# Kernel optimization log

Measured on AMD Instinct MI355X. Metric: run time of the kernel, lower is better.

Reference implementation:

```python
import jax, jax.numpy as jnp
import numpy as np

N = 50000   # input points
E = 800000  # edges
M = 25000   # sampled points (ratio 0.5)
K = 15      # num_neighbors
H = 128     # hidden_dim
BN_EPS = 1e-5


def setup_inputs() -> dict:
    key = jax.random.key(0)
    ks = jax.random.split(key, 16)
    w = lambda k, s: jax.random.normal(k, s, dtype=jnp.float32) * 0.02
    z = lambda s: jnp.zeros(s, jnp.float32)
    o = lambda s: jnp.ones(s, jnp.float32)
    return {
        'points': jax.random.normal(ks[0], (N, 3), jnp.float32),
        'edge_index': jax.random.randint(ks[1], (2, E), 0, N),
        'sampled_idx': jnp.sort(jax.random.randint(ks[2], (M,), 0, N)),
        'neighbors': jax.random.randint(ks[3], (M, K), 0, M),
        'W1': w(ks[4], (3, H)), 'b1': z(H), 'g1': o(H), 'beta1': z(H),
        'W2': w(ks[5], (H, H)), 'b2': z(H), 'g2': o(H), 'beta2': z(H),
        'Wc': w(ks[6], (H, H)), 'bc': z(H),
        'Wn': w(ks[7], (H, H)), 'bn_b': z(H),
        'Wq': w(ks[8], (H, H // 2)), 'bq': z(H // 2),
        'Wk': w(ks[9], (H, H // 2)), 'bk': z(H // 2),
        'Wcat': w(ks[10], (H + 3, H + 3)), 'bcat': z(H + 3),
        'Wout': w(ks[11], (H + 3, 3)), 'bout': z(3),
    }


def _bn(x, g, b):
    # BatchNorm1d in training mode: batch mean, biased batch var
    m = x.mean(axis=0)
    v = x.var(axis=0)
    return g * (x - m) * jax.lax.rsqrt(v + BN_EPS) + b


def reference(points, edge_index, sampled_idx, neighbors,
              W1, b1, g1, beta1, W2, b2, g2, beta2,
              Wc, bc, Wn, bn_b, Wq, bq, Wk, bk, Wcat, bcat, Wout, bout):
    n = points.shape[0]
    # PointMLP x2: Linear -> BN -> ReLU
    x = jax.nn.relu(_bn(points @ W1 + b1, g1, beta1))
    x = jax.nn.relu(_bn(x @ W2 + b2, g2, beta2))
    # CustomGNN: relu(W_c x + mean_{j in N(i)} W_n x_j)
    src, dst = edge_index[0], edge_index[1]
    msg = (x @ Wn + bn_b)[src]                                   # [E, H]
    agg = jax.ops.segment_sum(msg, dst, num_segments=n)          # [N, H]
    cnt = jax.ops.segment_sum(jnp.ones(src.shape, jnp.float32), dst, num_segments=n)
    agg = agg / jnp.maximum(cnt, 1.0)[:, None]
    x = jax.nn.relu(x @ Wc + bc + agg)
    # sampling (indices precomputed, like fps output)
    sp = points[sampled_idx]                                     # [M, 3]
    sx = x[sampled_idx]                                          # [M, H]
    # AttentionLayer, fully vectorized over sampled points
    q = sx @ Wq + bq                                             # [M, H/2]
    nb_x = sx[neighbors]                                         # [M, K, H]
    k = nb_x @ Wk + bk                                           # [M, K, H/2]
    scale = jnp.sqrt(jnp.float32(q.shape[-1])) + 1e-6
    scores = jnp.einsum('md,mkd->mk', q, k) / scale              # [M, K]
    mask = (neighbors != 0).astype(jnp.float32)                  # quirk preserved
    attn = jax.nn.softmax(scores * mask, axis=1)                 # [M, K]
    rel = sp[neighbors] - sp[:, None, :]                         # [M, K, 3]
    cat = jnp.concatenate([nb_x, rel], axis=-1)                  # [M, K, H+3]
    proc = cat @ Wcat + bcat                                     # [M, K, H+3]
    aggf = jnp.einsum('mk,mkd->md', attn, proc)                  # [M, H+3]
    disp = aggf @ Wout + bout                                    # [M, 3]
    refined = sp + disp
    return refined, sx
```

## Files before the change

### kernel.cpp

```cpp
#include <hip/hip_runtime.h>
#include <climits>

#define NPTS 50000
#define NE   800000
#define MS   25000
#define KN   15
#define HD   128

__device__ __forceinline__ float wave_sum(float v) {
#pragma unroll
    for (int o = 32; o > 0; o >>= 1) v += __shfl_xor(v, o, 64);
    return v;
}

__launch_bounds__(256)
__global__ void prep_kernel(const float* __restrict__ Wq, const float* __restrict__ bq,
                            const float* __restrict__ Wk, const float* __restrict__ bk,
                            const float* __restrict__ Wcat, const float* __restrict__ bcat,
                            const float* __restrict__ Wout, const float* __restrict__ bout,
                            const float* __restrict__ Wc, const float* __restrict__ Wn,
                            float* __restrict__ Wqk, float* __restrict__ biasQK,
                            float* __restrict__ WcWn,
                            float* __restrict__ Wco128, float* __restrict__ w3, float* __restrict__ bco) {
    int b = blockIdx.x, tid = threadIdx.x;
    if (b < 64) {
        int i = b * 256 + tid;
        int k = i >> 7, c = i & 127;
        Wqk[i] = (c < 64) ? Wq[k * 64 + c] : Wk[k * 64 + (c - 64)];
    } else if (b < 192) {
        int i = (b - 64) * 256 + tid;
        int k = i >> 7, c = i & 127;
        WcWn[i] = (k < 128) ? Wc[k * 128 + c] : Wn[(k - 128) * 128 + c];
    } else if (b == 192) {
        if (tid < 128) biasQK[tid] = (tid < 64) ? bq[tid] : bk[tid - 64];
    } else {
        int wid = tid >> 6, lane = tid & 63;
        int out = (b - 193) * 4 + wid;
        if (out < 396) {
            int r = out / 3, j = out - r * 3;
            const float* src = (r < 131) ? &Wcat[r * 131] : bcat;
            float s = 0.f;
            s = fmaf(src[lane], Wout[lane * 3 + j], s);
            s = fmaf(src[lane + 64], Wout[(lane + 64) * 3 + j], s);
            if (lane < 3) s = fmaf(src[lane + 128], Wout[(lane + 128) * 3 + j], s);
            s = wave_sum(s);
            if (lane == 0) {
                if (r < 128) Wco128[r * 3 + j] = s;
                else if (r < 131) w3[(r - 128) * 3 + j] = s;
                else bco[j] = s + bout[j];
            }
        }
    }
}

__launch_bounds__(256)
__global__ void lin1_kernel(const float* __restrict__ pts, const float* __restrict__ W1,
                            const float* __restrict__ b1, float* __restrict__ y1,
                            float* __restrict__ psum, float* __restrict__ psq) {
    int c = threadIdx.x & 127;
    int half = threadIdx.x >> 7;
    int part = blockIdx.x * 2 + half;
    float w0 = W1[c], w1 = W1[128 + c], w2 = W1[256 + c], bb = b1[c];
    float s = 0.f, s2 = 0.f;
    int r0 = part * 25, r1 = r0 + 25; if (r1 > NPTS) r1 = NPTS;
    for (int r = r0; r < r1; ++r) {
        float p0 = pts[r * 3], p1 = pts[r * 3 + 1], p2 = pts[r * 3 + 2];
        float y = fmaf(p0, w0, fmaf(p1, w1, fmaf(p2, w2, bb)));
        y1[r * HD + c] = y;
        s += y; s2 = fmaf(y, y, s2);
    }
    psum[part * 128 + c] = s;
    psq[part * 128 + c] = s2;
}

__launch_bounds__(256)
__global__ void bn_fin_par(const float* __restrict__ psum, const float* __restrict__ psq, int nb,
                           const float* __restrict__ g, const float* __restrict__ beta,
                           float* __restrict__ tp) {
    int c = blockIdx.x;
    int t = threadIdx.x;
    float S = 0.f, S2 = 0.f;
    for (int b = t; b < nb; b += 256) {
        S += psum[b * 128 + c];
        S2 += psq[b * 128 + c];
    }
    S = wave_sum(S); S2 = wave_sum(S2);
    __shared__ float sA[4], sB[4];
    int wid = t >> 6, lane = t & 63;
    if (lane == 0) { sA[wid] = S; sB[wid] = S2; }
    __syncthreads();
    if (t == 0) {
        float Sa = sA[0] + sA[1] + sA[2] + sA[3];
        float Sb = sB[0] + sB[1] + sB[2] + sB[3];
        const float invN = 1.f / (float)NPTS;
        float mean = Sa * invN;
        float var = Sb * invN - mean * mean;
        float a = g[c] * rsqrtf(var + 1e-5f);
        tp[c] = a;
        tp[128 + c] = beta[c] - mean * a;
    }
}

#define FMA_BLOCK \
        { float av = a0.x; FMA4(0, w0) } { float av = a0.y; FMA4(0, w1) } \
        { float av = a0.z; FMA4(0, w2) } { float av = a0.w; FMA4(0, w3v) } \
        { float av = a1.x; FMA4(1, w0) } { float av = a1.y; FMA4(1, w1) } \
        { float av = a1.z; FMA4(1, w2) } { float av = a1.w; FMA4(1, w3v) } \
        { float av = a2.x; FMA4(2, w0) } { float av = a2.y; FMA4(2, w1) } \
        { float av = a2.z; FMA4(2, w2) } { float av = a2.w; FMA4(2, w3v) }
#define FMA4(ai, wv) \
        acc[ai][0] = fmaf(av, wv.x, acc[ai][0]); acc[ai][1] = fmaf(av, wv.y, acc[ai][1]); \
        acc[ai][2] = fmaf(av, wv.z, acc[ai][2]); acc[ai][3] = fmaf(av, wv.w, acc[ai][3]);

template <bool TRANS, bool STATS>
__launch_bounds__(256)
__global__ void gemm_bn(const float* __restrict__ A, int nrows,
                        const float* __restrict__ W, const float* __restrict__ bias,
                        const float* __restrict__ tp,
                        float* __restrict__ Out,
                        float* __restrict__ psum, float* __restrict__ psq) {
    __shared__ float As[48][68];
    __shared__ float Ws[64][64];
    int tid = threadIdx.x;
    int cb = blockIdx.x & 1, rb = blockIdx.x >> 1;
    int r0 = rb * 48;
    int tc = tid & 15, tr = tid >> 4;
    int tr3 = tr * 3;
    float acc[3][4] = {};

    for (int k0 = 0; k0 < 128; k0 += 64) {
        if (k0) __syncthreads();
        for (int i = tid; i < 48 * 16; i += 256) {
            int r = i >> 4, c4 = (i & 15) << 2;
            int gr = r0 + r;
            float4 v = make_float4(0.f, 0.f, 0.f, 0.f);
            if (gr < nrows) {
                v = *reinterpret_cast<const float4*>(&A[gr * HD + k0 + c4]);
                if (TRANS) {
                    int gc = k0 + c4;
                    v.x = fmaxf(fmaf(tp[gc],     v.x, tp[128 + gc]),     0.f);
                    v.y = fmaxf(fmaf(tp[gc + 1], v.y, tp[128 + gc + 1]), 0.f);
                    v.z = fmaxf(fmaf(tp[gc + 2], v.z, tp[128 + gc + 2]), 0.f);
                    v.w = fmaxf(fmaf(tp[gc + 3], v.w, tp[128 + gc + 3]), 0.f);
                }
            }
            *reinterpret_cast<float4*>(&As[r][c4]) = v;
        }
        for (int i = tid; i < 64 * 16; i += 256) {
            int k = i >> 4, c4 = (i & 15) << 2;
            *reinterpret_cast<float4*>(&Ws[k][c4]) =
                *reinterpret_cast<const float4*>(&W[(k0 + k) * 128 + (cb << 6) + c4]);
        }
        __syncthreads();
#pragma unroll 2
        for (int k = 0; k < 64; k += 4) {
            const float4 a0 = *reinterpret_cast<const float4*>(&As[tr3][k]);
            const float4 a1 = *reinterpret_cast<const float4*>(&As[tr3 + 1][k]);
            const float4 a2 = *reinterpret_cast<const float4*>(&As[tr3 + 2][k]);
            const float4 w0 = *reinterpret_cast<const float4*>(&Ws[k][tc << 2]);
            const float4 w1 = *reinterpret_cast<const float4*>(&Ws[k + 1][tc << 2]);
            const float4 w2 = *reinterpret_cast<const float4*>(&Ws[k + 2][tc << 2]);
            const float4 w3v = *reinterpret_cast<const float4*>(&Ws[k + 3][tc << 2]);
            FMA_BLOCK
        }
    }

    int c0 = (cb << 6) + (tc << 2);
    float b0 = bias[c0], b1v = bias[c0 + 1], b2v = bias[c0 + 2], b3v = bias[c0 + 3];
    float cs[4] = {}, cq[4] = {};
#pragma unroll
    for (int i = 0; i < 3; ++i) {
        int gr = r0 + tr3 + i;
        float v0 = acc[i][0] + b0, v1 = acc[i][1] + b1v, v2 = acc[i][2] + b2v, v3 = acc[i][3] + b3v;
        if (gr < nrows) {
            *reinterpret_cast<float4*>(&Out[gr * HD + c0]) = make_float4(v0, v1, v2, v3);
            if (STATS) {
                cs[0] += v0; cs[1] += v1; cs[2] += v2; cs[3] += v3;
                cq[0] = fmaf(v0, v0, cq[0]); cq[1] = fmaf(v1, v1, cq[1]);
                cq[2] = fmaf(v2, v2, cq[2]); cq[3] = fmaf(v3, v3, cq[3]);
            }
        }
    }
    if (STATS) {
        float* red = &As[0][0];
        __syncthreads();
        *reinterpret_cast<float4*>(&red[tr * 64 + (tc << 2)]) = make_float4(cs[0], cs[1], cs[2], cs[3]);
        __syncthreads();
        if (tid < 64) {
            float s = 0.f;
            for (int t = 0; t < 16; ++t) s += red[t * 64 + tid];
            psum[rb * 128 + (cb << 6) + tid] = s;
        }
        __syncthreads();
        *reinterpret_cast<float4*>(&red[tr * 64 + (tc << 2)]) = make_float4(cq[0], cq[1], cq[2], cq[3]);
        __syncthreads();
        if (tid < 64) {
            float s = 0.f;
            for (int t = 0; t < 16; ++t) s += red[t * 64 + tid];
            psq[rb * 128 + (cb << 6) + tid] = s;
        }
    }
}

__launch_bounds__(256)
__global__ void init_kernel(int* __restrict__ inv, int* __restrict__ cnt, int* __restrict__ cursor) {
    int i = blockIdx.x * 256 + threadIdx.x;
    if (i < NPTS) inv[i] = INT_MAX;
    if (i < MS) { cnt[i] = 0; cursor[i] = 0; }
}

__launch_bounds__(256)
__global__ void invset_kernel(const int* __restrict__ smp, int* __restrict__ inv) {
    int m = blockIdx.x * 256 + threadIdx.x;
    if (m < MS) atomicMin(&inv[smp[m]], m);
}

__launch_bounds__(256)
__global__ void count_kernel(const int* __restrict__ ei, const int* __restrict__ inv,
                             int* __restrict__ cnt) {
    int e = blockIdx.x * 256 + threadIdx.x;
    if (e < NE) {
        int mr = inv[ei[NE + e]];
        if (mr < MS) atomicAdd(&cnt[mr], 1);
    }
}

__launch_bounds__(1024)
__global__ void scan_kernel(const int* __restrict__ cnt, int* __restrict__ offs) {
    const int C = 25;
    __shared__ int buf[1024];
    int tid = threadIdx.x;
    int loc[C];
    int run = 0;
    int base = tid * C;
#pragma unroll
    for (int i = 0; i < C; ++i) {
        int idx = base + i;
        int v = (idx < MS) ? cnt[idx] : 0;
        loc[i] = run; run += v;
    }
    buf[tid] = run;
    __syncthreads();
    for (int off = 1; off < 1024; off <<= 1) {
        int t = (tid >= off) ? buf[tid - off] : 0;
        __syncthreads();
        buf[tid] += t;
        __syncthreads();
    }
    int excl = buf[tid] - run;
#pragma unroll
    for (int i = 0; i < C; ++i) {
        int idx = base + i;
        if (idx < MS) offs[idx] = excl + loc[i];
    }
    if (tid == 1023) offs[MS] = buf[tid];
}

__launch_bounds__(256)
__global__ void scatter_kernel(const int* __restrict__ ei, const int* __restrict__ inv,
                               const int* __restrict__ offs, int* __restrict__ cursor,
                               int* __restrict__ elist) {
    int e = blockIdx.x * 256 + threadIdx.x;
    if (e < NE) {
        int mr = inv[ei[NE + e]];
        if (mr < MS) {
            int pos = atomicAdd(&cursor[mr], 1);
            elist[offs[mr] + pos] = ei[e];
        }
    }
}

__launch_bounds__(256)
__global__ void agg_kernel(const int* __restrict__ smp, const int* __restrict__ inv,
                           const int* __restrict__ offs, const int* __restrict__ elist,
                           const float* __restrict__ y2, const float* __restrict__ tp2,
                           float* __restrict__ aggX, float* __restrict__ hasE) {
    int tid = threadIdx.x, wid = tid >> 6, lane = tid & 63;
    int m = blockIdx.x * 4 + wid;
    if (m >= MS) return;
    int d = smp[m];
    if (inv[d] != m) return;
    int c0 = lane << 1;
    float ta0 = tp2[c0], ta1 = tp2[c0 + 1];
    float tb0 = tp2[128 + c0], tb1 = tp2[128 + c0 + 1];
    int e0 = offs[m], e1 = offs[m + 1];
    float sx0[8] = {}, sx1[8] = {};
    int e = e0;
    for (; e + 7 < e1; e += 8) {
        float2 v[8];
#pragma unroll
        for (int j = 0; j < 8; ++j)
            v[j] = *reinterpret_cast<const float2*>(&y2[elist[e + j] * HD + c0]);
#pragma unroll
        for (int j = 0; j < 8; ++j) {
            sx0[j] += fmaxf(fmaf(ta0, v[j].x, tb0), 0.f);
            sx1[j] += fmaxf(fmaf(ta1, v[j].y, tb1), 0.f);
        }
    }
    for (; e < e1; ++e) {
        const float2 v = *reinterpret_cast<const float2*>(&y2[elist[e] * HD + c0]);
        sx0[0] += fmaxf(fmaf(ta0, v.x, tb0), 0.f);
        sx1[0] += fmaxf(fmaf(ta1, v.y, tb1), 0.f);
    }
    float s0 = ((sx0[0] + sx0[1]) + (sx0[2] + sx0[3])) + ((sx0[4] + sx0[5]) + (sx0[6] + sx0[7]));
    float s1 = ((sx1[0] + sx1[1]) + (sx1[2] + sx1[3])) + ((sx1[4] + sx1[5]) + (sx1[6] + sx1[7]));
    float rs = 1.f / fmaxf((float)(e1 - e0), 1.f);
    *reinterpret_cast<float2*>(&aggX[m * HD + c0]) = make_float2(s0 * rs, s1 * rs);
    if (lane == 0) hasE[m] = (e1 > e0) ? 1.f : 0.f;
}

__launch_bounds__(256)
__global__ void gemm_sx(const float* __restrict__ y2, const float* __restrict__ aggX,
                        const float* __restrict__ hasE,
                        const int* __restrict__ smp, const int* __restrict__ inv,
                        const float* __restrict__ WcWn,
                        const float* __restrict__ bc, const float* __restrict__ bn_b,
                        const float* __restrict__ tp2,
                        float* __restrict__ sx) {
    __shared__ float As[48][68];
    __shared__ float Ws[64][64];
    int tid = threadIdx.x;
    int cb = blockIdx.x & 1, rb = blockIdx.x >> 1;
    int r0 = rb * 48;
    int tc = tid & 15, tr = tid >> 4;
    int tr3 = tr * 3;
    float acc[3][4] = {};

    for (int kk = 0; kk < 4; ++kk) {
        if (kk) __syncthreads();
        for (int i = tid; i < 48 * 16; i += 256) {
            int r = i >> 4, c4 = (i & 15) << 2;
            int gr = r0 + r;
            float4 v = make_float4(0.f, 0.f, 0.f, 0.f);
            if (gr < MS) {
                int d = smp[gr];
                if (kk < 2) {
                    int gc = (kk << 6) + c4;
                    v = *reinterpret_cast<const float4*>(&y2[d * HD + gc]);
                    v.x = fmaxf(fmaf(tp2[gc],     v.x, tp2[128 + gc]),     0.f);
                    v.y = fmaxf(fmaf(tp2[gc + 1], v.y, tp2[128 + gc + 1]), 0.f);
                    v.z = fmaxf(fmaf(tp2[gc + 2], v.z, tp2[128 + gc + 2]), 0.f);
                    v.w = fmaxf(fmaf(tp2[gc + 3], v.w, tp2[128 + gc + 3]), 0.f);
                } else {
                    v = *reinterpret_cast<const float4*>(&aggX[inv[d] * HD + ((kk - 2) << 6) + c4]);
                }
            }
            *reinterpret_cast<float4*>(&As[r][c4]) = v;
        }
        for (int i = tid; i < 64 * 16; i += 256) {
            int k = i >> 4, c4 = (i & 15) << 2;
            *reinterpret_cast<float4*>(&Ws[k][c4]) =
                *reinterpret_cast<const float4*>(&WcWn[((kk << 6) + k) * 128 + (cb << 6) + c4]);
        }
        __syncthreads();
#pragma unroll 2
        for (int k = 0; k < 64; k += 4) {
            const float4 a0 = *reinterpret_cast<const float4*>(&As[tr3][k]);
            const float4 a1 = *reinterpret_cast<const float4*>(&As[tr3 + 1][k]);
            const float4 a2 = *reinterpret_cast<const float4*>(&As[tr3 + 2][k]);
            const float4 w0 = *reinterpret_cast<const float4*>(&Ws[k][tc << 2]);
            const float4 w1 = *reinterpret_cast<const float4*>(&Ws[k + 1][tc << 2]);
            const float4 w2 = *reinterpret_cast<const float4*>(&Ws[k + 2][tc << 2]);
            const float4 w3v = *reinterpret_cast<const float4*>(&Ws[k + 3][tc << 2]);
            FMA_BLOCK
        }
    }

    int c0 = (cb << 6) + (tc << 2);
    float4 bcv = *reinterpret_cast<const float4*>(&bc[c0]);
    float4 bnv = *reinterpret_cast<const float4*>(&bn_b[c0]);
#pragma unroll
    for (int i = 0; i < 3; ++i) {
        int gr = r0 + tr3 + i;
        if (gr < MS) {
            float f = hasE[inv[smp[gr]]];
            float v0 = fmaxf(acc[i][0] + bcv.x + f * bnv.x, 0.f);
            float v1 = fmaxf(acc[i][1] + bcv.y + f * bnv.y, 0.f);
            float v2 = fmaxf(acc[i][2] + bcv.z + f * bnv.z, 0.f);
            float v3 = fmaxf(acc[i][3] + bcv.w + f * bnv.w, 0.f);
            *reinterpret_cast<float4*>(&sx[gr * HD + c0]) = make_float4(v0, v1, v2, v3);
        }
    }
}

__launch_bounds__(256)
__global__ void p3_kernel(const float* __restrict__ sx, const float* __restrict__ Wco128,
                          const int* __restrict__ smp, const float* __restrict__ pts,
                          float* __restrict__ p3, float* __restrict__ sp) {
    int wid = threadIdx.x >> 6, lane = threadIdx.x & 63;
    int m = blockIdx.x * 4 + wid;
    if (m >= MS) return;
    int c0 = lane << 1;
    const float2 v = *reinterpret_cast<const float2*>(&sx[m * HD + c0]);
    float q0 = v.x * Wco128[c0 * 3]     + v.y * Wco128[(c0 + 1) * 3];
    float q1 = v.x * Wco128[c0 * 3 + 1] + v.y * Wco128[(c0 + 1) * 3 + 1];
    float q2 = v.x * Wco128[c0 * 3 + 2] + v.y * Wco128[(c0 + 1) * 3 + 2];
    q0 = wave_sum(q0); q1 = wave_sum(q1); q2 = wave_sum(q2);
    int d = smp[m];
    if (lane == 0) { p3[m * 3] = q0; p3[m * 3 + 1] = q1; p3[m * 3 + 2] = q2; }
    if (lane < 3) sp[m * 3 + lane] = pts[d * 3 + lane];
}

__launch_bounds__(256)
__global__ void attn_kernel(const float* __restrict__ qk, const int* __restrict__ nbr,
                            const float* __restrict__ p3, const float* __restrict__ sp,
                            const float* __restrict__ w3, const float* __restrict__ bco,
                            float* __restrict__ refined) {
    int wid = threadIdx.x >> 6, lane = threadIdx.x & 63;
    int m = blockIdx.x * 4 + wid;
    if (m >= MS) return;
    float ql = qk[m * HD + lane];
    int nbv[KN];
    float s[KN];
#pragma unroll
    for (int j = 0; j < KN; ++j) nbv[j] = nbr[m * KN + j];
#pragma unroll
    for (int j = 0; j < KN; ++j) {
        float t = ql * qk[nbv[j] * HD + 64 + lane];
        t = wave_sum(t);
        s[j] = (nbv[j] != 0) ? t * (1.f / 8.000001f) : 0.f;
    }
    float mx = s[0];
#pragma unroll
    for (int j = 1; j < KN; ++j) mx = fmaxf(mx, s[j]);
    float den = 0.f;
#pragma unroll
    for (int j = 0; j < KN; ++j) { s[j] = __expf(s[j] - mx); den += s[j]; }
    float invd = 1.f / den;
    float sp0 = sp[m * 3], sp1 = sp[m * 3 + 1], sp2 = sp[m * 3 + 2];
    float a0 = 0.f, a1 = 0.f, a2 = 0.f;
#pragma unroll
    for (int j = 0; j < KN; ++j) {
        int nb = nbv[j];
        float wgt = s[j] * invd;
        float r0 = sp[nb * 3] - sp0, r1 = sp[nb * 3 + 1] - sp1, r2 = sp[nb * 3 + 2] - sp2;
        float g0 = p3[nb * 3]     + r0 * w3[0] + r1 * w3[3] + r2 * w3[6];
        float g1 = p3[nb * 3 + 1] + r0 * w3[1] + r1 * w3[4] + r2 * w3[7];
        float g2 = p3[nb * 3 + 2] + r0 * w3[2] + r1 * w3[5] + r2 * w3[8];
        a0 = fmaf(wgt, g0, a0); a1 = fmaf(wgt, g1, a1); a2 = fmaf(wgt, g2, a2);
    }
    if (lane == 0) {
        refined[m * 3]     = sp0 + a0 + bco[0];
        refined[m * 3 + 1] = sp1 + a1 + bco[1];
        refined[m * 3 + 2] = sp2 + a2 + bco[2];
    }
}

extern "C" void kernel_launch(void* const* d_in, const int* in_sizes, int n_in,
                              void* d_out, int out_size, void* d_ws, size_t ws_size,
                              hipStream_t stream) {
    const float* pts   = (const float*)d_in[0];
    const int*   ei    = (const int*)d_in[1];
    const int*   smp   = (const int*)d_in[2];
    const int*   nbr   = (const int*)d_in[3];
    const float* W1    = (const float*)d_in[4];
    const float* b1    = (const float*)d_in[5];
    const float* g1    = (const float*)d_in[6];
    const float* beta1 = (const float*)d_in[7];
    const float* W2    = (const float*)d_in[8];
    const float* b2    = (const float*)d_in[9];
    const float* g2    = (const float*)d_in[10];
    const float* beta2 = (const float*)d_in[11];
    const float* Wc    = (const float*)d_in[12];
    const float* bc    = (const float*)d_in[13];
    const float* Wn    = (const float*)d_in[14];
    const float* bn_b  = (const float*)d_in[15];
    const float* Wq    = (const float*)d_in[16];
    const float* bq    = (const float*)d_in[17];
    const float* Wk    = (const float*)d_in[18];
    const float* bk    = (const float*)d_in[19];
    const float* Wcat  = (const float*)d_in[20];
    const float* bcat  = (const float*)d_in[21];
    const float* Wout  = (const float*)d_in[22];
    const float* bout  = (const float*)d_in[23];
    (void)in_sizes; (void)n_in; (void)out_size; (void)ws_size;

    float* w = (float*)d_ws;
    size_t o = 0;
    float* y1     = w + o; o += 6400000;
    float* y2     = w + o; o += 6400000;
    float* aggX   = w + o; o += 3200000;
    float* qkb    = w + o; o += 3200000;
    float* psum   = w + o; o += 262144;
    float* psq    = w + o; o += 262144;
    float* tp1    = w + o; o += 256;
    float* tp2    = w + o; o += 256;
    float* Wqk    = w + o; o += 16384;
    float* biasQK = w + o; o += 128;
    float* WcWn   = w + o; o += 32768;
    float* Wco128 = w + o; o += 384;
    float* w3     = w + o; o += 16;
    float* bco    = w + o; o += 16;
    float* p3     = w + o; o += 75008;
    float* sp     = w + o; o += 75008;
    float* hasE   = w + o; o += 25008;
    int* ip    = (int*)(w + o);
    int* inv   = ip;            ip += NPTS;
    int* cnt   = ip;            ip += MS;
    int* cursor= ip;            ip += MS;
    int* offs  = ip;            ip += MS + 4;
    int* elist = ip;

    float* refined = (float*)d_out;
    float* sx      = (float*)d_out + 75000;

    prep_kernel<<<292, 256, 0, stream>>>(Wq, bq, Wk, bk, Wcat, bcat, Wout, bout, Wc, Wn,
                                         Wqk, biasQK, WcWn, Wco128, w3, bco);
    lin1_kernel<<<1000, 256, 0, stream>>>(pts, W1, b1, y1, psum, psq);
    bn_fin_par<<<128, 256, 0, stream>>>(psum, psq, 2000, g1, beta1, tp1);
    gemm_bn<true, true><<<2084, 256, 0, stream>>>(y1, NPTS, W2, b2, tp1, y2, psum, psq);
    bn_fin_par<<<128, 256, 0, stream>>>(psum, psq, 1042, g2, beta2, tp2);
    init_kernel<<<196, 256, 0, stream>>>(inv, cnt, cursor);
    invset_kernel<<<98, 256, 0, stream>>>(smp, inv);
    count_kernel<<<3125, 256, 0, stream>>>(ei, inv, cnt);
    scan_kernel<<<1, 1024, 0, stream>>>(cnt, offs);
    scatter_kernel<<<3125, 256, 0, stream>>>(ei, inv, offs, cursor, elist);
    agg_kernel<<<6250, 256, 0, stream>>>(smp, inv, offs, elist, y2, tp2, aggX, hasE);
    gemm_sx<<<1042, 256, 0, stream>>>(y2, aggX, hasE, smp, inv, WcWn, bc, bn_b, tp2, sx);
    p3_kernel<<<6250, 256, 0, stream>>>(sx, Wco128, smp, pts, p3, sp);
    gemm_bn<false, false><<<1042, 256, 0, stream>>>(sx, MS, Wqk, biasQK, nullptr, qkb,
                                                    nullptr, nullptr);
    attn_kernel<<<6250, 256, 0, stream>>>(qkb, nbr, p3, sp, w3, bco, refined);
}
```

Before: 337.6 us.

## Fuse index-setup kernels into compute launches, widen GEMM tiles, vectorize aggregation

Three small setup kernels are removed by folding their work into extra blocks of existing launches. Buffer init moves into prep_kernel, inverse-map atomicMin into lin1_kernel, and edge counting into the first BN GEMM. The GEMM kernels now compute all 128 output columns per block instead of splitting columns across two blocks, which halves grid size and reuses A tiles at the cost of more registers and LDS. The aggregation kernel splits each wave into two half-waves that each load float4 rows for alternating edges and combine them with a shuffle, improving memory access width.

```diff
diff --git a/kernel.cpp b/kernel.cpp
--- a/kernel.cpp
+++ b/kernel.cpp
@@ -21,7 +21,8 @@
                             const float* __restrict__ Wc, const float* __restrict__ Wn,
                             float* __restrict__ Wqk, float* __restrict__ biasQK,
                             float* __restrict__ WcWn,
-                            float* __restrict__ Wco128, float* __restrict__ w3, float* __restrict__ bco) {
+                            float* __restrict__ Wco128, float* __restrict__ w3, float* __restrict__ bco,
+                            int* __restrict__ inv, int* __restrict__ cnt, int* __restrict__ cursor) {
     int b = blockIdx.x, tid = threadIdx.x;
     if (b < 64) {
         int i = b * 256 + tid;
@@ -33,7 +34,7 @@
         WcWn[i] = (k < 128) ? Wc[k * 128 + c] : Wn[(k - 128) * 128 + c];
     } else if (b == 192) {
         if (tid < 128) biasQK[tid] = (tid < 64) ? bq[tid] : bk[tid - 64];
-    } else {
+    } else if (b < 293) {
         int wid = tid >> 6, lane = tid & 63;
         int out = (b - 193) * 4 + wid;
         if (out < 396) {
@@ -50,13 +51,23 @@
                 else bco[j] = s + bout[j];
             }
         }
+    } else {
+        int i = (b - 293) * 256 + tid;
+        if (i < NPTS) inv[i] = INT_MAX;
+        if (i < MS) { cnt[i] = 0; cursor[i] = 0; }
     }
 }
 
 __launch_bounds__(256)
 __global__ void lin1_kernel(const float* __restrict__ pts, const float* __restrict__ W1,
                             const float* __restrict__ b1, float* __restrict__ y1,
-                            float* __restrict__ psum, float* __restrict__ psq) {
+                            float* __restrict__ psum, float* __restrict__ psq,
+                            const int* __restrict__ smp, int* __restrict__ inv) {
+    if (blockIdx.x >= 1000) {
+        int m = (blockIdx.x - 1000) * 256 + threadIdx.x;
+        if (m < MS) atomicMin(&inv[smp[m]], m);
+        return;
+    }
     int c = threadIdx.x & 127;
     int half = threadIdx.x >> 7;
     int part = blockIdx.x * 2 + half;
@@ -101,32 +112,30 @@
     }
 }
 
-#define FMA_BLOCK \
-        { float av = a0.x; FMA4(0, w0) } { float av = a0.y; FMA4(0, w1) } \
-        { float av = a0.z; FMA4(0, w2) } { float av = a0.w; FMA4(0, w3v) } \
-        { float av = a1.x; FMA4(1, w0) } { float av = a1.y; FMA4(1, w1) } \
-        { float av = a1.z; FMA4(1, w2) } { float av = a1.w; FMA4(1, w3v) } \
-        { float av = a2.x; FMA4(2, w0) } { float av = a2.y; FMA4(2, w1) } \
-        { float av = a2.z; FMA4(2, w2) } { float av = a2.w; FMA4(2, w3v) }
-#define FMA4(ai, wv) \
-        acc[ai][0] = fmaf(av, wv.x, acc[ai][0]); acc[ai][1] = fmaf(av, wv.y, acc[ai][1]); \
-        acc[ai][2] = fmaf(av, wv.z, acc[ai][2]); acc[ai][3] = fmaf(av, wv.w, acc[ai][3]);
-
-template <bool TRANS, bool STATS>
-__launch_bounds__(256)
-__global__ void gemm_bn(const float* __restrict__ A, int nrows,
+template <bool TRANS, bool STATS, bool COUNT>
+__launch_bounds__(256)
+__global__ void gemm_bn(const float* __restrict__ A, int nrows, int gemmBlocks,
                         const float* __restrict__ W, const float* __restrict__ bias,
                         const float* __restrict__ tp,
                         float* __restrict__ Out,
-                        float* __restrict__ psum, float* __restrict__ psq) {
+                        float* __restrict__ psum, float* __restrict__ psq,
+                        const int* __restrict__ ei, const int* __restrict__ inv,
+                        int* __restrict__ cnt) {
+    if (COUNT && (int)blockIdx.x >= gemmBlocks) {
+        int e = ((int)blockIdx.x - gemmBlocks) * 256 + threadIdx.x;
+        if (e < NE) {
+            int mr = inv[ei[NE + e]];
+            if (mr < MS) atomicAdd(&cnt[mr], 1);
+        }
+        return;
+    }
     __shared__ float As[48][68];
-    __shared__ float Ws[64][64];
+    __shared__ float Ws[64][128];
     int tid = threadIdx.x;
-    int cb = blockIdx.x & 1, rb = blockIdx.x >> 1;
-    int r0 = rb * 48;
+    int r0 = blockIdx.x * 48;
     int tc = tid & 15, tr = tid >> 4;
-    int tr3 = tr * 3;
-    float acc[3][4] = {};
+    int tr3 = tr * 3, tc8 = tc << 3;
+    float accA[3][4] = {}, accB[3][4] = {};
 
     for (int k0 = 0; k0 < 128; k0 += 64) {
         if (k0) __syncthreads();
@@ -146,10 +155,10 @@
             }
             *reinterpret_cast<float4*>(&As[r][c4]) = v;
         }
-        for (int i = tid; i < 64 * 16; i += 256) {
-            int k = i >> 4, c4 = (i & 15) << 2;
+        for (int i = tid; i < 64 * 32; i += 256) {
+            int k = i >> 5, c4 = (i & 31) << 2;
             *reinterpret_cast<float4*>(&Ws[k][c4]) =
-                *reinterpret_cast<const float4*>(&W[(k0 + k) * 128 + (cb << 6) + c4]);
+                *reinterpret_cast<const float4*>(&W[(k0 + k) * 128 + c4]);
         }
         __syncthreads();
 #pragma unroll 2
@@ -157,71 +166,73 @@
             const float4 a0 = *reinterpret_cast<const float4*>(&As[tr3][k]);
             const float4 a1 = *reinterpret_cast<const float4*>(&As[tr3 + 1][k]);
             const float4 a2 = *reinterpret_cast<const float4*>(&As[tr3 + 2][k]);
-            const float4 w0 = *reinterpret_cast<const float4*>(&Ws[k][tc << 2]);
-            const float4 w1 = *reinterpret_cast<const float4*>(&Ws[k + 1][tc << 2]);
-            const float4 w2 = *reinterpret_cast<const float4*>(&Ws[k + 2][tc << 2]);
-            const float4 w3v = *reinterpret_cast<const float4*>(&Ws[k + 3][tc << 2]);
-            FMA_BLOCK
-        }
-    }
-
-    int c0 = (cb << 6) + (tc << 2);
-    float b0 = bias[c0], b1v = bias[c0 + 1], b2v = bias[c0 + 2], b3v = bias[c0 + 3];
-    float cs[4] = {}, cq[4] = {};
+            float a0v[4] = {a0.x, a0.y, a0.z, a0.w};
+            float a1v[4] = {a1.x, a1.y, a1.z, a1.w};
+            float a2v[4] = {a2.x, a2.y, a2.z, a2.w};
+#pragma unroll
+            for (int kk = 0; kk < 4; ++kk) {
+                const float4 wlo = *reinterpret_cast<const float4*>(&Ws[k + kk][tc8]);
+                const float4 whi = *reinterpret_cast<const float4*>(&Ws[k + kk][tc8 + 4]);
+                float v0 = a0v[kk], v1 = a1v[kk], v2 = a2v[kk];
+                accA[0][0] = fmaf(v0, wlo.x, accA[0][0]); accA[0][1] = fmaf(v0, wlo.y, accA[0][1]);
+                accA[0][2] = fmaf(v0, wlo.z, accA[0][2]); accA[0][3] = fmaf(v0, wlo.w, accA[0][3]);
+                accB[0][0] = fmaf(v0, whi.x, accB[0][0]); accB[0][1] = fmaf(v0, whi.y, accB[0][1]);
+                accB[0][2] = fmaf(v0, whi.z, accB[0][2]); accB[0][3] = fmaf(v0, whi.w, accB[0][3]);
+                accA[1][0] = fmaf(v1, wlo.x, accA[1][0]); accA[1][1] = fmaf(v1, wlo.y, accA[1][1]);
+                accA[1][2] = fmaf(v1, wlo.z, accA[1][2]); accA[1][3] = fmaf(v1, wlo.w, accA[1][3]);
+                accB[1][0] = fmaf(v1, whi.x, accB[1][0]); accB[1][1] = fmaf(v1, whi.y, accB[1][1]);
+                accB[1][2] = fmaf(v1, whi.z, accB[1][2]); accB[1][3] = fmaf(v1, whi.w, accB[1][3]);
+                accA[2][0] = fmaf(v2, wlo.x, accA[2][0]); accA[2][1] = fmaf(v2, wlo.y, accA[2][1]);
+                accA[2][2] = fmaf(v2, wlo.z, accA[2][2]); accA[2][3] = fmaf(v2, wlo.w, accA[2][3]);
+                accB[2][0] = fmaf(v2, whi.x, accB[2][0]); accB[2][1] = fmaf(v2, whi.y, accB[2][1]);
+                accB[2][2] = fmaf(v2, whi.z, accB[2][2]); accB[2][3] = fmaf(v2, whi.w, accB[2][3]);
+            }
+        }
+    }
+
+    const float4 blo = *reinterpret_cast<const float4*>(&bias[tc8]);
+    const float4 bhi = *reinterpret_cast<const float4*>(&bias[tc8 + 4]);
+    float cs[8] = {}, cq[8] = {};
 #pragma unroll
     for (int i = 0; i < 3; ++i) {
         int gr = r0 + tr3 + i;
-        float v0 = acc[i][0] + b0, v1 = acc[i][1] + b1v, v2 = acc[i][2] + b2v, v3 = acc[i][3] + b3v;
+        float o0 = accA[i][0] + blo.x, o1 = accA[i][1] + blo.y;
+        float o2 = accA[i][2] + blo.z, o3 = accA[i][3] + blo.w;
+        float o4 = accB[i][0] + bhi.x, o5 = accB[i][1] + bhi.y;
+        float o6 = accB[i][2] + bhi.z, o7 = accB[i][3] + bhi.w;
         if (gr < nrows) {
-            *reinterpret_cast<float4*>(&Out[gr * HD + c0]) = make_float4(v0, v1, v2, v3);
+            *reinterpret_cast<float4*>(&Out[gr * HD + tc8])     = make_float4(o0, o1, o2, o3);
+            *reinterpret_cast<float4*>(&Out[gr * HD + tc8 + 4]) = make_float4(o4, o5, o6, o7);
             if (STATS) {
-                cs[0] += v0; cs[1] += v1; cs[2] += v2; cs[3] += v3;
-                cq[0] = fmaf(v0, v0, cq[0]); cq[1] = fmaf(v1, v1, cq[1]);
-                cq[2] = fmaf(v2, v2, cq[2]); cq[3] = fmaf(v3, v3, cq[3]);
+                cs[0] += o0; cs[1] += o1; cs[2] += o2; cs[3] += o3;
+                cs[4] += o4; cs[5] += o5; cs[6] += o6; cs[7] += o7;
+                cq[0] = fmaf(o0, o0, cq[0]); cq[1] = fmaf(o1, o1, cq[1]);
+                cq[2] = fmaf(o2, o2, cq[2]); cq[3] = fmaf(o3, o3, cq[3]);
+                cq[4] = fmaf(o4, o4, cq[4]); cq[5] = fmaf(o5, o5, cq[5]);
+                cq[6] = fmaf(o6, o6, cq[6]); cq[7] = fmaf(o7, o7, cq[7]);
             }
         }
     }
     if (STATS) {
         float* red = &As[0][0];
         __syncthreads();
-        *reinterpret_cast<float4*>(&red[tr * 64 + (tc << 2)]) = make_float4(cs[0], cs[1], cs[2], cs[3]);
-        __syncthreads();
-        if (tid < 64) {
+        *reinterpret_cast<float4*>(&red[tr * 128 + tc8])     = make_float4(cs[0], cs[1], cs[2], cs[3]);
+        *reinterpret_cast<float4*>(&red[tr * 128 + tc8 + 4]) = make_float4(cs[4], cs[5], cs[6], cs[7]);
+        __syncthreads();
+        if (tid < 128) {
             float s = 0.f;
-            for (int t = 0; t < 16; ++t) s += red[t * 64 + tid];
-            psum[rb * 128 + (cb << 6) + tid] = s;
-        }
-        __syncthreads();
-        *reinterpret_cast<float4*>(&red[tr * 64 + (tc << 2)]) = make_float4(cq[0], cq[1], cq[2], cq[3]);
-        __syncthreads();
-        if (tid < 64) {
+            for (int t = 0; t < 16; ++t) s += red[t * 128 + tid];
+            psum[blockIdx.x * 128 + tid] = s;
+        }
+        __syncthreads();
+        *reinterpret_cast<float4*>(&red[tr * 128 + tc8])     = make_float4(cq[0], cq[1], cq[2], cq[3]);
+        *reinterpret_cast<float4*>(&red[tr * 128 + tc8 + 4]) = make_float4(cq[4], cq[5], cq[6], cq[7]);
+        __syncthreads();
+        if (tid < 128) {
             float s = 0.f;
-            for (int t = 0; t < 16; ++t) s += red[t * 64 + tid];
-            psq[rb * 128 + (cb << 6) + tid] = s;
-        }
-    }
-}
-
-__launch_bounds__(256)
-__global__ void init_kernel(int* __restrict__ inv, int* __restrict__ cnt, int* __restrict__ cursor) {
-    int i = blockIdx.x * 256 + threadIdx.x;
-    if (i < NPTS) inv[i] = INT_MAX;
-    if (i < MS) { cnt[i] = 0; cursor[i] = 0; }
-}
-
-__launch_bounds__(256)
-__global__ void invset_kernel(const int* __restrict__ smp, int* __restrict__ inv) {
-    int m = blockIdx.x * 256 + threadIdx.x;
-    if (m < MS) atomicMin(&inv[smp[m]], m);
-}
-
-__launch_bounds__(256)
-__global__ void count_kernel(const int* __restrict__ ei, const int* __restrict__ inv,
-                             int* __restrict__ cnt) {
-    int e = blockIdx.x * 256 + threadIdx.x;
-    if (e < NE) {
-        int mr = inv[ei[NE + e]];
-        if (mr < MS) atomicAdd(&cnt[mr], 1);
+            for (int t = 0; t < 16; ++t) s += red[t * 128 + tid];
+            psq[blockIdx.x * 128 + tid] = s;
+        }
     }
 }
 
@@ -280,32 +291,45 @@
     if (m >= MS) return;
     int d = smp[m];
     if (inv[d] != m) return;
-    int c0 = lane << 1;
-    float ta0 = tp2[c0], ta1 = tp2[c0 + 1];
-    float tb0 = tp2[128 + c0], tb1 = tp2[128 + c0 + 1];
+    int half = lane >> 5, c0 = (lane & 31) << 2;
+    const float4 ta = *reinterpret_cast<const float4*>(&tp2[c0]);
+    const float4 tb = *reinterpret_cast<const float4*>(&tp2[128 + c0]);
     int e0 = offs[m], e1 = offs[m + 1];
-    float sx0[8] = {}, sx1[8] = {};
+    float4 s0 = {0,0,0,0}, s1 = {0,0,0,0}, s2 = {0,0,0,0}, s3 = {0,0,0,0};
     int e = e0;
     for (; e + 7 < e1; e += 8) {
-        float2 v[8];
-#pragma unroll
-        for (int j = 0; j < 8; ++j)
-            v[j] = *reinterpret_cast<const float2*>(&y2[elist[e + j] * HD + c0]);
-#pragma unroll
-        for (int j = 0; j < 8; ++j) {
-            sx0[j] += fmaxf(fmaf(ta0, v[j].x, tb0), 0.f);
-            sx1[j] += fmaxf(fmaf(ta1, v[j].y, tb1), 0.f);
-        }
-    }
-    for (; e < e1; ++e) {
-        const float2 v = *reinterpret_cast<const float2*>(&y2[elist[e] * HD + c0]);
-        sx0[0] += fmaxf(fmaf(ta0, v.x, tb0), 0.f);
-        sx1[0] += fmaxf(fmaf(ta1, v.y, tb1), 0.f);
-    }
-    float s0 = ((sx0[0] + sx0[1]) + (sx0[2] + sx0[3])) + ((sx0[4] + sx0[5]) + (sx0[6] + sx0[7]));
-    float s1 = ((sx1[0] + sx1[1]) + (sx1[2] + sx1[3])) + ((sx1[4] + sx1[5]) + (sx1[6] + sx1[7]));
+        float4 v[4];
+#pragma unroll
+        for (int u = 0; u < 4; ++u)
+            v[u] = *reinterpret_cast<const float4*>(&y2[elist[e + 2 * u + half] * HD + c0]);
+        s0.x += fmaxf(fmaf(ta.x, v[0].x, tb.x), 0.f); s0.y += fmaxf(fmaf(ta.y, v[0].y, tb.y), 0.f);
+        s0.z += fmaxf(fmaf(ta.z, v[0].z, tb.z), 0.f); s0.w += fmaxf(fmaf(ta.w, v[0].w, tb.w), 0.f);
+        s1.x += fmaxf(fmaf(ta.x, v[1].x, tb.x), 0.f); s1.y += fmaxf(fmaf(ta.y, v[1].y, tb.y), 0.f);
+        s1.z += fmaxf(fmaf(ta.z, v[1].z, tb.z), 0.f); s1.w += fmaxf(fmaf(ta.w, v[1].w, tb.w), 0.f);
+        s2.x += fmaxf(fmaf(ta.x, v[2].x, tb.x), 0.f); s2.y += fmaxf(fmaf(ta.y, v[2].y, tb.y), 0.f);
+        s2.z += fmaxf(fmaf(ta.z, v[2].z, tb.z), 0.f); s2.w += fmaxf(fmaf(ta.w, v[2].w, tb.w), 0.f);
+        s3.x += fmaxf(fmaf(ta.x, v[3].x, tb.x), 0.f); s3.y += fmaxf(fmaf(ta.y, v[3].y, tb.y), 0.f);
+        s3.z += fmaxf(fmaf(ta.z, v[3].z, tb.z), 0.f); s3.w += fmaxf(fmaf(ta.w, v[3].w, tb.w), 0.f);
+    }
+    for (; e + 1 < e1; e += 2) {
+        const float4 v = *reinterpret_cast<const float4*>(&y2[elist[e + half] * HD + c0]);
+        s0.x += fmaxf(fmaf(ta.x, v.x, tb.x), 0.f); s0.y += fmaxf(fmaf(ta.y, v.y, tb.y), 0.f);
+        s0.z += fmaxf(fmaf(ta.z, v.z, tb.z), 0.f); s0.w += fmaxf(fmaf(ta.w, v.w, tb.w), 0.f);
+    }
+    if (e < e1 && half == 0) {
+        const float4 v = *reinterpret_cast<const float4*>(&y2[elist[e] * HD + c0]);
+        s1.x += fmaxf(fmaf(ta.x, v.x, tb.x), 0.f); s1.y += fmaxf(fmaf(ta.y, v.y, tb.y), 0.f);
+        s1.z += fmaxf(fmaf(ta.z, v.z, tb.z), 0.f); s1.w += fmaxf(fmaf(ta.w, v.w, tb.w), 0.f);
+    }
+    float tx = (s0.x + s1.x) + (s2.x + s3.x);
+    float ty = (s0.y + s1.y) + (s2.y + s3.y);
+    float tz = (s0.z + s1.z) + (s2.z + s3.z);
+    float tw = (s0.w + s1.w) + (s2.w + s3.w);
+    tx += __shfl_xor(tx, 32, 64); ty += __shfl_xor(ty, 32, 64);
+    tz += __shfl_xor(tz, 32, 64); tw += __shfl_xor(tw, 32, 64);
     float rs = 1.f / fmaxf((float)(e1 - e0), 1.f);
-    *reinterpret_cast<float2*>(&aggX[m * HD + c0]) = make_float2(s0 * rs, s1 * rs);
+    if (half == 0)
+        *reinterpret_cast<float4*>(&aggX[m * HD + c0]) = make_float4(tx * rs, ty * rs, tz * rs, tw * rs);
     if (lane == 0) hasE[m] = (e1 > e0) ? 1.f : 0.f;
 }
 
@@ -318,13 +342,12 @@
                         const float* __restrict__ tp2,
                         float* __restrict__ sx) {
     __shared__ float As[48][68];
-    __shared__ float Ws[64][64];
+    __shared__ float Ws[64][128];
     int tid = threadIdx.x;
-    int cb = blockIdx.x & 1, rb = blockIdx.x >> 1;
-    int r0 = rb * 48;
+    int r0 = blockIdx.x * 48;
     int tc = tid & 15, tr = tid >> 4;
-    int tr3 = tr * 3;
-    float acc[3][4] = {};
+    int tr3 = tr * 3, tc8 = tc << 3;
+    float accA[3][4] = {}, accB[3][4] = {};
 
     for (int kk = 0; kk < 4; ++kk) {
         if (kk) __syncthreads();
@@ -347,10 +370,10 @@
             }
             *reinterpret_cast<float4*>(&As[r][c4]) = v;
         }
-        for (int i = tid; i < 64 * 16; i += 256) {
-            int k = i >> 4, c4 = (i & 15) << 2;
+        for (int i = tid; i < 64 * 32; i += 256) {
+            int k = i >> 5, c4 = (i & 31) << 2;
             *reinterpret_cast<float4*>(&Ws[k][c4]) =
-                *reinterpret_cast<const float4*>(&WcWn[((kk << 6) + k) * 128 + (cb << 6) + c4]);
+                *reinterpret_cast<const float4*>(&WcWn[((kk << 6) + k) * 128 + c4]);
         }
         __syncthreads();
 #pragma unroll 2
@@ -358,27 +381,49 @@
             const float4 a0 = *reinterpret_cast<const float4*>(&As[tr3][k]);
             const float4 a1 = *reinterpret_cast<const float4*>(&As[tr3 + 1][k]);
             const float4 a2 = *reinterpret_cast<const float4*>(&As[tr3 + 2][k]);
-            const float4 w0 = *reinterpret_cast<const float4*>(&Ws[k][tc << 2]);
-            const float4 w1 = *reinterpret_cast<const float4*>(&Ws[k + 1][tc << 2]);
-            const float4 w2 = *reinterpret_cast<const float4*>(&Ws[k + 2][tc << 2]);
-            const float4 w3v = *reinterpret_cast<const float4*>(&Ws[k + 3][tc << 2]);
-            FMA_BLOCK
-        }
-    }
-
-    int c0 = (cb << 6) + (tc << 2);
-    float4 bcv = *reinterpret_cast<const float4*>(&bc[c0]);
-    float4 bnv = *reinterpret_cast<const float4*>(&bn_b[c0]);
+            float a0v[4] = {a0.x, a0.y, a0.z, a0.w};
+            float a1v[4] = {a1.x, a1.y, a1.z, a1.w};
+            float a2v[4] = {a2.x, a2.y, a2.z, a2.w};
+#pragma unroll
+            for (int kq = 0; kq < 4; ++kq) {
+                const float4 wlo = *reinterpret_cast<const float4*>(&Ws[k + kq][tc8]);
+                const float4 whi = *reinterpret_cast<const float4*>(&Ws[k + kq][tc8 + 4]);
+                float v0 = a0v[kq], v1 = a1v[kq], v2 = a2v[kq];
+                accA[0][0] = fmaf(v0, wlo.x, accA[0][0]); accA[0][1] = fmaf(v0, wlo.y, accA[0][1]);
+                accA[0][2] = fmaf(v0, wlo.z, accA[0][2]); accA[0][3] = fmaf(v0, wlo.w, accA[0][3]);
+                accB[0][0] = fmaf(v0, whi.x, accB[0][0]); accB[0][1] = fmaf(v0, whi.y, accB[0][1]);
+                accB[0][2] = fmaf(v0, whi.z, accB[0][2]); accB[0][3] = fmaf(v0, whi.w, accB[0][3]);
+                accA[1][0] = fmaf(v1, wlo.x, accA[1][0]); accA[1][1] = fmaf(v1, wlo.y, accA[1][1]);
+                accA[1][2] = fmaf(v1, wlo.z, accA[1][2]); accA[1][3] = fmaf(v1, wlo.w, accA[1][3]);
+                accB[1][0] = fmaf(v1, whi.x, accB[1][0]); accB[1][1] = fmaf(v1, whi.y, accB[1][1]);
+                accB[1][2] = fmaf(v1, whi.z, accB[1][2]); accB[1][3] = fmaf(v1, whi.w, accB[1][3]);
+                accA[2][0] = fmaf(v2, wlo.x, accA[2][0]); accA[2][1] = fmaf(v2, wlo.y, accA[2][1]);
+                accA[2][2] = fmaf(v2, wlo.z, accA[2][2]); accA[2][3] = fmaf(v2, wlo.w, accA[2][3]);
+                accB[2][0] = fmaf(v2, whi.x, accB[2][0]); accB[2][1] = fmaf(v2, whi.y, accB[2][1]);
+                accB[2][2] = fmaf(v2, whi.z, accB[2][2]); accB[2][3] = fmaf(v2, whi.w, accB[2][3]);
+            }
+        }
+    }
+
+    const float4 bclo = *reinterpret_cast<const float4*>(&bc[tc8]);
+    const float4 bchi = *reinterpret_cast<const float4*>(&bc[tc8 + 4]);
+    const float4 bnlo = *reinterpret_cast<const float4*>(&bn_b[tc8]);
+    const float4 bnhi = *reinterpret_cast<const float4*>(&bn_b[tc8 + 4]);
 #pragma unroll
     for (int i = 0; i < 3; ++i) {
         int gr = r0 + tr3 + i;
         if (gr < MS) {
             float f = hasE[inv[smp[gr]]];
-            float v0 = fmaxf(acc[i][0] + bcv.x + f * bnv.x, 0.f);
-            float v1 = fmaxf(acc[i][1] + bcv.y + f * bnv.y, 0.f);
-            float v2 = fmaxf(acc[i][2] + bcv.z + f * bnv.z, 0.f);
-            float v3 = fmaxf(acc[i][3] + bcv.w + f * bnv.w, 0.f);
-            *reinterpret_cast<float4*>(&sx[gr * HD + c0]) = make_float4(v0, v1, v2, v3);
+            float o0 = fmaxf(accA[i][0] + bclo.x + f * bnlo.x, 0.f);
+            float o1 = fmaxf(accA[i][1] + bclo.y + f * bnlo.y, 0.f);
+            float o2 = fmaxf(accA[i][2] + bclo.z + f * bnlo.z, 0.f);
+            float o3 = fmaxf(accA[i][3] + bclo.w + f * bnlo.w, 0.f);
+            float o4 = fmaxf(accB[i][0] + bchi.x + f * bnhi.x, 0.f);
+            float o5 = fmaxf(accB[i][1] + bchi.y + f * bnhi.y, 0.f);
+            float o6 = fmaxf(accB[i][2] + bchi.z + f * bnhi.z, 0.f);
+            float o7 = fmaxf(accB[i][3] + bchi.w + f * bnhi.w, 0.f);
+            *reinterpret_cast<float4*>(&sx[gr * HD + tc8])     = make_float4(o0, o1, o2, o3);
+            *reinterpret_cast<float4*>(&sx[gr * HD + tc8 + 4]) = make_float4(o4, o5, o6, o7);
         }
     }
 }
@@ -504,21 +549,20 @@
     float* refined = (float*)d_out;
     float* sx      = (float*)d_out + 75000;
 
-    prep_kernel<<<292, 256, 0, stream>>>(Wq, bq, Wk, bk, Wcat, bcat, Wout, bout, Wc, Wn,
-                                         Wqk, biasQK, WcWn, Wco128, w3, bco);
-    lin1_kernel<<<1000, 256, 0, stream>>>(pts, W1, b1, y1, psum, psq);
+    prep_kernel<<<489, 256, 0, stream>>>(Wq, bq, Wk, bk, Wcat, bcat, Wout, bout, Wc, Wn,
+                                         Wqk, biasQK, WcWn, Wco128, w3, bco,
+                                         inv, cnt, cursor);
+    lin1_kernel<<<1098, 256, 0, stream>>>(pts, W1, b1, y1, psum, psq, smp, inv);
     bn_fin_par<<<128, 256, 0, stream>>>(psum, psq, 2000, g1, beta1, tp1);
-    gemm_bn<true, true><<<2084, 256, 0, stream>>>(y1, NPTS, W2, b2, tp1, y2, psum, psq);
+    gemm_bn<true, true, true><<<1042 + 3125, 256, 0, stream>>>(
+        y1, NPTS, 1042, W2, b2, tp1, y2, psum, psq, ei, inv, cnt);
     bn_fin_par<<<128, 256, 0, stream>>>(psum, psq, 1042, g2, beta2, tp2);
-    init_kernel<<<196, 256, 0, stream>>>(inv, cnt, cursor);
-    invset_kernel<<<98, 256, 0, stream>>>(smp, inv);
-    count_kernel<<<3125, 256, 0, stream>>>(ei, inv, cnt);
     scan_kernel<<<1, 1024, 0, stream>>>(cnt, offs);
     scatter_kernel<<<3125, 256, 0, stream>>>(ei, inv, offs, cursor, elist);
     agg_kernel<<<6250, 256, 0, stream>>>(smp, inv, offs, elist, y2, tp2, aggX, hasE);
-    gemm_sx<<<1042, 256, 0, stream>>>(y2, aggX, hasE, smp, inv, WcWn, bc, bn_b, tp2, sx);
+    gemm_sx<<<521, 256, 0, stream>>>(y2, aggX, hasE, smp, inv, WcWn, bc, bn_b, tp2, sx);
     p3_kernel<<<6250, 256, 0, stream>>>(sx, Wco128, smp, pts, p3, sp);
-    gemm_bn<false, false><<<1042, 256, 0, stream>>>(sx, MS, Wqk, biasQK, nullptr, qkb,
-                                                    nullptr, nullptr);
+    gemm_bn<false, false, false><<<521, 256, 0, stream>>>(
+        sx, MS, 521, Wqk, biasQK, nullptr, qkb, nullptr, nullptr, nullptr, nullptr, nullptr);
     attn_kernel<<<6250, 256, 0, stream>>>(qkb, nbr, p3, sp, w3, bco, refined);
 }
```

Result: no change. 334.6 us (-0.9%).
